# Kernel tuning notes

Hardware: AMD Instinct MI355X
Metric: run time of the kernel (lower is better)

Reference implementation:

```python
import jax, jax.numpy as jnp
import numpy as np

DIM = 2048
NUM_HEADS = 16
HEAD_DIM = 128
SEQ = 4096
HDIM = NUM_HEADS * HEAD_DIM
EPS = 1e-6


def _rope_tables(seq_len, head_dim):
    quarter = head_dim // 4
    ang = (1.0 / 1024.0) ** np.linspace(0.0, 1.0, quarter, dtype=np.float32)
    ang = np.concatenate([ang, np.zeros(quarter, dtype=np.float32)])  # [head_dim//2]
    theta = np.arange(seq_len, dtype=np.float32)[:, None] * ang[None, :]  # [T, D/2]
    return jnp.asarray(np.cos(theta)), jnp.asarray(np.sin(theta))


def _rms_norm(x):
    return x * jax.lax.rsqrt(jnp.mean(x * x, axis=-1, keepdims=True) + EPS)


def _apply_rope(x, cos, sin):
    # x: [B, T, H, D]; cos/sin: [T, D/2]
    c = cos[None, :, None, :]
    s = sin[None, :, None, :]
    x1, x2 = jnp.split(x, 2, axis=-1)
    return jnp.concatenate([x1 * c + x2 * s, -x1 * s + x2 * c], axis=-1)


def setup_inputs() -> dict:
    key = jax.random.key(0)
    k1, k2, k3, k4, k5 = jax.random.split(key, 5)
    x = jax.random.normal(k1, (1, SEQ, DIM), dtype=jnp.float32)
    ve = jax.random.normal(k2, (1, SEQ, HDIM), dtype=jnp.float32)
    lambdas = jax.random.uniform(k3, (2,), dtype=jnp.float32)
    bound = (3.0 ** 0.5) * 0.5 * DIM ** (-0.5)
    qkv_w = jax.random.uniform(k4, (3, HDIM, DIM), dtype=jnp.float32, minval=-bound, maxval=bound)
    proj_w = 0.02 * jax.random.normal(k5, (DIM, HDIM), dtype=jnp.float32)
    return {"x": x, "ve": ve, "lambdas": lambdas, "qkv_w": qkv_w, "proj_w": proj_w}


def reference(x, ve, lambdas, qkv_w, proj_w):
    B, T, _ = x.shape
    cos, sin = _rope_tables(T, HEAD_DIM)
    # fused QKV projection: qkv_w [3, hdim, dim]
    qkv = jnp.einsum('btd,ced->cbte', x, qkv_w)  # [3, B, T, hdim]
    q, k, v = [a.reshape(B, T, NUM_HEADS, HEAD_DIM) for a in qkv]
    q = _apply_rope(_rms_norm(q), cos, sin)
    k = _apply_rope(_rms_norm(k), cos, sin)
    v = lambdas[0] * v + lambdas[1] * ve.reshape(v.shape)
    # causal SDPA, default scale 1/sqrt(head_dim)
    scale = 1.0 / jnp.sqrt(jnp.float32(HEAD_DIM))
    scores = jnp.einsum('bthd,bshd->bhts', q, k) * scale  # [B, H, T, T]
    causal = jnp.tril(jnp.ones((T, T), dtype=bool))
    scores = jnp.where(causal[None, None], scores, jnp.float32(-1e30))
    probs = jax.nn.softmax(scores, axis=-1)
    out = jnp.einsum('bhts,bshd->bthd', probs, v).reshape(B, T, HDIM)
    return out @ proj_w.T
```

## Files before the change

### kernel.cpp

```cpp
#include <hip/hip_runtime.h>
#include <cstdint>
#include <cstddef>

constexpr int T_SEQ = 4096;
constexpr int NH    = 16;
constexpr int HD    = 128;
constexpr int DIM   = 2048;
constexpr int HDIM  = 2048;

typedef __attribute__((ext_vector_type(8)))  short  short8;
typedef __attribute__((ext_vector_type(4)))  float  f32x4;
typedef __attribute__((ext_vector_type(16))) float  f32x16;
typedef __attribute__((ext_vector_type(8)))  unsigned short u16x8;
typedef __attribute__((ext_vector_type(4)))  unsigned short u16x4;
typedef __attribute__((ext_vector_type(4)))  unsigned uint4v;
typedef __attribute__((ext_vector_type(2)))  int int2v;

__device__ __forceinline__ unsigned short f2bf(float f) {
  unsigned u = __float_as_uint(f);
  return (unsigned short)((u + 0x7FFFu + ((u >> 16) & 1u)) >> 16);
}
__device__ __forceinline__ float bf2f(unsigned short h) {
  return __uint_as_float(((unsigned)h) << 16);
}
__device__ __forceinline__ void gload_lds16(const void* g, void* l) {
  __builtin_amdgcn_global_load_lds((const __attribute__((address_space(1))) void*)g,
                                   (__attribute__((address_space(3))) void*)l, 16, 0, 0);
}
__device__ __forceinline__ int2v plswap(int a, int b) {
  return __builtin_amdgcn_permlane32_swap(a, b, false, false);
}
__device__ __forceinline__ void bar() {
  asm volatile("" ::: "memory");
  __builtin_amdgcn_s_barrier();
  asm volatile("" ::: "memory");
}
#define VMCNT(n) asm volatile("s_waitcnt vmcnt(" #n ")" ::: "memory")

__global__ __launch_bounds__(256) void cvt_f32_bf16(const float* __restrict__ in,
                                                    unsigned short* __restrict__ out, int n4) {
  int i = blockIdx.x * 256 + threadIdx.x;
  if (i < n4) {
    float4 v = ((const float4*)in)[i];
    u16x4 o; o.x = f2bf(v.x); o.y = f2bf(v.y); o.z = f2bf(v.z); o.w = f2bf(v.w);
    ((u16x4*)out)[i] = o;
  }
}

__global__ __launch_bounds__(256) void rope_tables(float* __restrict__ cosT, float* __restrict__ sinT) {
  int idx = blockIdx.x * 256 + threadIdx.x;
  if (idx >= T_SEQ * 64) return;
  int t = idx >> 6, i = idx & 63;
  float ang = (i < 32) ? exp2f(-10.0f * (float)i / 31.0f) : 0.0f;
  float th = (float)t * ang;
  cosT[idx] = cosf(th);
  sinT[idx] = sinf(th);
}

template <int MODE>
__global__ __launch_bounds__(512) void gemm256(const unsigned short* __restrict__ A,
                                               const unsigned short* __restrict__ B,
                                               int K, unsigned short* __restrict__ outb,
                                               float* __restrict__ outf, int N) {
  __shared__ __align__(16) char SM[3 * 49152];
  const int tid = threadIdx.x, w = tid >> 6, lane = tid & 63;
  const int wm = w >> 2, wn = w & 3;
  const int lr = lane >> 4, lc = lane & 15, lc7 = lc & 7;
  const int cpx = gridDim.x >> 3;
  const int idx = (blockIdx.x & 7) * cpx + (blockIdx.x >> 3);
  const int m0 = (idx & 31) * 128, n0 = (idx >> 5) * 256;

  const int arow = lane >> 3;
  const int xcol = ((lane & 7) ^ ((lane >> 3) & 7)) * 8;

  auto stageA = [&](int buf, int t) {
    char* base = SM + buf * 49152;
#pragma unroll
    for (int i = 0; i < 2; i++) {
      int c = w + i * 8;
      gload_lds16(A + (size_t)(m0 + c * 8 + arow) * K + t * 64 + xcol, base + c * 1024);
    }
  };
  auto stageB0 = [&](int buf, int t) {
    char* base = SM + buf * 49152 + 16384;
    gload_lds16(B + (size_t)(n0 + w * 8 + arow) * K + t * 64 + xcol, base + w * 1024);
  };
  auto stageB1 = [&](int buf, int t) {
    char* base = SM + buf * 49152 + 16384;
#pragma unroll
    for (int i = 1; i < 4; i++) {
      int c = w + i * 8;
      gload_lds16(B + (size_t)(n0 + c * 8 + arow) * K + t * 64 + xcol, base + c * 1024);
    }
  };

  f32x4 acc[4][4] = {};
  const int NT = K >> 6;

  stageA(0, 0); stageB0(0, 0); stageB1(0, 0);
  stageA(1, 1); stageB0(1, 1); stageB1(1, 1);
  VMCNT(6);
  bar();

#pragma unroll 1
  for (int t = 0; t < NT; t++) {
    const int c = t % 3, s = (t + 2) % 3;
    const bool st = (t + 2) < NT;
    const char* Ab = SM + c * 49152;
    const char* Bb = Ab + 16384;

    short8 a[4], b[4];
#pragma unroll
    for (int mi = 0; mi < 4; mi++)
      a[mi] = *(const short8*)(Ab + (wm * 64 + mi * 16 + lc) * 128 + ((0 + lr) ^ lc7) * 16);
#pragma unroll
    for (int ni = 0; ni < 4; ni++)
      b[ni] = *(const short8*)(Bb + (wn * 64 + ni * 16 + lc) * 128 + ((0 + lr) ^ lc7) * 16);
    if (st) { stageA(s, t + 2); stageB0(s, t + 2); }
    bar();
    __builtin_amdgcn_s_setprio(1);
#pragma unroll
    for (int mi = 0; mi < 4; mi++)
#pragma unroll
      for (int ni = 0; ni < 4; ni++)
        acc[mi][ni] = __builtin_amdgcn_mfma_f32_16x16x32_bf16(a[mi], b[ni], acc[mi][ni], 0, 0, 0);
    __builtin_amdgcn_s_setprio(0);
    bar();

#pragma unroll
    for (int mi = 0; mi < 4; mi++)
      a[mi] = *(const short8*)(Ab + (wm * 64 + mi * 16 + lc) * 128 + ((4 + lr) ^ lc7) * 16);
#pragma unroll
    for (int ni = 0; ni < 4; ni++)
      b[ni] = *(const short8*)(Bb + (wn * 64 + ni * 16 + lc) * 128 + ((4 + lr) ^ lc7) * 16);
    if (st) stageB1(s, t + 2);
    if (st) { VMCNT(6); } else { VMCNT(0); }
    bar();
    __builtin_amdgcn_s_setprio(1);
#pragma unroll
    for (int mi = 0; mi < 4; mi++)
#pragma unroll
      for (int ni = 0; ni < 4; ni++)
        acc[mi][ni] = __builtin_amdgcn_mfma_f32_16x16x32_bf16(a[mi], b[ni], acc[mi][ni], 0, 0, 0);
    __builtin_amdgcn_s_setprio(0);
    bar();
  }

#pragma unroll
  for (int mi = 0; mi < 4; mi++)
#pragma unroll
    for (int ni = 0; ni < 4; ni++)
#pragma unroll
      for (int r = 0; r < 4; r++) {
        int t = m0 + wm * 64 + mi * 16 + lr * 4 + r;
        int n = n0 + wn * 64 + ni * 16 + lc;
        float v = acc[mi][ni][r];
        if (MODE == 0) {
          int cc = n >> 11, e = n & 2047, h = e >> 7, d = e & 127;
          outb[(((size_t)cc * NH + h) * T_SEQ + t) * HD + d] = f2bf(v);
        } else {
          outf[(size_t)t * N + n] = v;
        }
      }
}

__global__ __launch_bounds__(256) void norm_rope(unsigned short* __restrict__ qkvb,
                                                 const float* __restrict__ cosT,
                                                 const float* __restrict__ sinT) {
  const int tid = threadIdx.x;
  const int li = tid & 15;
  const int row = blockIdx.x * 16 + (tid >> 4);
  const int t = row & (T_SEQ - 1);
  unsigned short* rp = qkvb + (size_t)row * HD + li * 8;
  u16x8 raw = *(const u16x8*)rp;

  float v[8]; float ss = 0.0f;
#pragma unroll
  for (int j = 0; j < 8; j++) { v[j] = bf2f(raw[j]); ss += v[j] * v[j]; }
#pragma unroll
  for (int off = 1; off < 16; off <<= 1) ss += __shfl_xor(ss, off, 16);
  float rs = rsqrtf(ss * (1.0f / 128.0f) + 1e-6f);
  if (row < NH * T_SEQ) rs *= 0.088388347648318447f * 1.44269504f;

  uint4v rw = __builtin_bit_cast(uint4v, raw);
  uint4v pwv;
  pwv.x = (unsigned)__shfl_xor((int)rw.x, 8, 16);
  pwv.y = (unsigned)__shfl_xor((int)rw.y, 8, 16);
  pwv.z = (unsigned)__shfl_xor((int)rw.z, 8, 16);
  pwv.w = (unsigned)__shfl_xor((int)rw.w, 8, 16);
  u16x8 praw = __builtin_bit_cast(u16x8, pwv);
  float pv[8];
#pragma unroll
  for (int j = 0; j < 8; j++) pv[j] = bf2f(praw[j]);

  const int e0 = (li & 7) * 8;
  const bool hi8 = li >= 8;
  float4 c0 = *(const float4*)(cosT + t * 64 + e0);
  float4 c1 = *(const float4*)(cosT + t * 64 + e0 + 4);
  float4 s0 = *(const float4*)(sinT + t * 64 + e0);
  float4 s1 = *(const float4*)(sinT + t * 64 + e0 + 4);
  float cc[8] = {c0.x, c0.y, c0.z, c0.w, c1.x, c1.y, c1.z, c1.w};
  float sn[8] = {s0.x, s0.y, s0.z, s0.w, s1.x, s1.y, s1.z, s1.w};

  u16x8 o;
#pragma unroll
  for (int j = 0; j < 8; j++) {
    float x1 = hi8 ? pv[j] : v[j];
    float x2 = hi8 ? v[j] : pv[j];
    float r = hi8 ? (-x1 * sn[j] + x2 * cc[j]) : (x1 * cc[j] + x2 * sn[j]);
    o[j] = f2bf(r * rs);
  }
  *(u16x8*)rp = o;
}

__global__ __launch_bounds__(256) void vmix_transpose(const unsigned short* __restrict__ vb,
                                                      const float* __restrict__ ve,
                                                      const float* __restrict__ lam,
                                                      unsigned short* __restrict__ vt) {
  __shared__ float tile[64][65];
  const int h = blockIdx.z, t0 = blockIdx.x * 64, d0 = blockIdx.y * 64;
  const float l0 = lam[0], l1 = lam[1];
  const int tid = threadIdx.x;
  const int tl = tid >> 4, dl4 = (tid & 15) * 4;
#pragma unroll
  for (int i = 0; i < 4; i++) {
    int t_local = tl + i * 16;
    int t = t0 + t_local;
    const unsigned short* vp = vb + ((size_t)h * T_SEQ + t) * HD + d0 + dl4;
    const float* vep = ve + (size_t)t * HDIM + h * HD + d0 + dl4;
    u16x4 vv = *(const u16x4*)vp;
    float4 vef = *(const float4*)vep;
    tile[t_local][dl4 + 0] = l0 * bf2f(vv.x) + l1 * vef.x;
    tile[t_local][dl4 + 1] = l0 * bf2f(vv.y) + l1 * vef.y;
    tile[t_local][dl4 + 2] = l0 * bf2f(vv.z) + l1 * vef.z;
    tile[t_local][dl4 + 3] = l0 * bf2f(vv.w) + l1 * vef.w;
  }
  __syncthreads();
#pragma unroll
  for (int i = 0; i < 2; i++) {
    int idx = tid + i * 256;
    int d_local = idx >> 3, tloc = (idx & 7) * 8;
    u16x8 o;
#pragma unroll
    for (int j = 0; j < 8; j++) o[j] = f2bf(tile[tloc + j][d_local]);
    *(u16x8*)(vt + ((size_t)h * HD + d0 + d_local) * T_SEQ + t0 + tloc) = o;
  }
}

__global__ __launch_bounds__(512)
__attribute__((amdgpu_waves_per_eu(2, 2)))
void attn_fwd(const unsigned short* __restrict__ qb,
              const unsigned short* __restrict__ kb,
              const unsigned short* __restrict__ vt,
              unsigned short* __restrict__ ao) {
  __shared__ __align__(16) char SMEM[131072];
  __shared__ int gctr[2];
  const int bid = blockIdx.x;
  const int h  = (bid & 7) + ((bid >> 7) << 3);
  const int pr = (bid >> 3) & 15;
  const int tid = threadIdx.x, w = tid >> 6, lane = tid & 63;
  const int g = w >> 2, wq = w & 3;
  const int l31 = lane & 31, hi = lane >> 5, r7 = l31 & 7;
  const unsigned short* qh = qb + (size_t)h * T_SEQ * HD;
  const unsigned short* kh = kb + (size_t)h * T_SEQ * HD;
  const unsigned short* vh = vt + (size_t)h * HD * T_SEQ;

  if (tid < 2) gctr[tid] = 0;
  __syncthreads();
  int bcnt = 0;
  auto GBAR = [&]() {
    asm volatile("s_waitcnt lgkmcnt(0)" ::: "memory");
    ++bcnt;
    if (lane == 0)
      __hip_atomic_fetch_add(&gctr[g], 1, __ATOMIC_RELEASE, __HIP_MEMORY_SCOPE_WORKGROUP);
    while (__hip_atomic_load(&gctr[g], __ATOMIC_ACQUIRE, __HIP_MEMORY_SCOPE_WORKGROUP) < 4 * bcnt)
      __builtin_amdgcn_s_sleep(1);
  };

  char* Kbase = SMEM + g * 65536;
  char* Vbase = SMEM + g * 65536 + 32768;

  const int kcrow = lane >> 4, kcol16 = lane & 15;
  const int vcrow = lane >> 3, vslot0 = lane & 7;

  auto STAGE = [&](int buf, int t) {
#pragma unroll
    for (int i = 0; i < 4; i++) {
      int krow = (wq * 4 + i) * 4 + kcrow;
      int kcol = (kcol16 ^ (krow & 7)) * 8;
      gload_lds16(kh + (size_t)(t * 64 + krow) * HD + kcol,
                  Kbase + buf * 16384 + (wq * 4 + i) * 1024);
      int vrow = (wq * 4 + i) * 8 + vcrow;
      int vcol = (vslot0 ^ (vrow & 7)) * 8;
      gload_lds16(vh + (size_t)vrow * T_SEQ + t * 64 + vcol,
                  Vbase + buf * 16384 + (wq * 4 + i) * 1024);
    }
  };

  const float FM = 16.5f;

#pragma unroll 1
  for (int which = 0; which < 2; ++which) {
    const int qt = which ? pr : (31 - pr);
    const int ng = qt + 1;
    const int q_row = qt * 128 + wq * 32 + l31;

    short8 qf[8];
#pragma unroll
    for (int dk = 0; dk < 8; dk++)
      qf[dk] = *(const short8*)(qh + (size_t)q_row * HD + dk * 16 + hi * 8);

    f32x16 accO[4] = {};
    float l_r = 0.0f;

    __syncthreads();
    STAGE(0, g);

#pragma unroll 1
    for (int it = 0; it < ng; it++) {
      const int t = 2 * it + g;
      const int cur = it & 1;
      asm volatile("s_waitcnt vmcnt(0)" ::: "memory");
      GBAR();
      if (it + 1 < ng) STAGE(cur ^ 1, t + 2);

      f32x16 accS0 = {}, accS1 = {};
      const char* Kb = Kbase + cur * 16384 + l31 * 256;
      __builtin_amdgcn_s_setprio(1);
#pragma unroll
      for (int dk = 0; dk < 8; dk++) {
        int sl = ((2 * dk + hi) ^ r7) * 16;
        short8 k0 = *(const short8*)(Kb + sl);
        short8 k1 = *(const short8*)(Kb + 32 * 256 + sl);
        accS0 = __builtin_amdgcn_mfma_f32_32x32x16_bf16(k0, qf[dk], accS0, 0, 0, 0);
        accS1 = __builtin_amdgcn_mfma_f32_32x32x16_bf16(k1, qf[dk], accS1, 0, 0, 0);
      }
      __builtin_amdgcn_s_setprio(0);

      float p[32];
      const bool need_mask = (t * 64 + 63) > (qt * 128 + wq * 32);
      if (need_mask) {
#pragma unroll
        for (int r = 0; r < 16; r++) {
          int kv0 = t * 64 + (r & 3) + 8 * (r >> 2) + 4 * hi;
          p[r]      = (kv0      > q_row) ? 0.0f : exp2f(accS0[r] - FM);
          p[16 + r] = (kv0 + 32 > q_row) ? 0.0f : exp2f(accS1[r] - FM);
        }
      } else {
#pragma unroll
        for (int r = 0; r < 16; r++) {
          p[r]      = exp2f(accS0[r] - FM);
          p[16 + r] = exp2f(accS1[r] - FM);
        }
      }

      float s16[16];
#pragma unroll
      for (int i = 0; i < 16; i++) s16[i] = p[i] + p[i + 16];
#pragma unroll
      for (int st = 8; st >= 1; st >>= 1)
#pragma unroll
        for (int i = 0; i < st; i++) s16[i] += s16[i + st];
      int2v sr_ = plswap(__float_as_int(s16[0]), __float_as_int(s16[0]));
      l_r += s16[0] + __int_as_float(hi ? sr_.x : sr_.y);

      unsigned pk[8][2];
#pragma unroll
      for (int o = 0; o < 8; o++)
#pragma unroll
        for (int c = 0; c < 2; c++) {
          float lo = p[(o >> 2) * 16 + (o & 3) * 4 + 2 * c];
          float hi_ = p[(o >> 2) * 16 + (o & 3) * 4 + 2 * c + 1];
          asm("v_cvt_pk_bf16_f32 %0, %1, %2" : "=v"(pk[o][c]) : "v"(lo), "v"(hi_));
        }

      const char* Vb = Vbase + cur * 16384 + l31 * 128;
#pragma unroll
      for (int ks = 0; ks < 4; ks++) {
        int2v s0 = plswap((int)pk[2 * ks][0], (int)pk[2 * ks + 1][0]);
        int2v s1 = plswap((int)pk[2 * ks][1], (int)pk[2 * ks + 1][1]);
        uint4v pw;
        pw.x = (unsigned)s0.x;
        pw.y = (unsigned)s1.x;
        pw.z = (unsigned)s0.y;
        pw.w = (unsigned)s1.y;
        short8 pb = __builtin_bit_cast(short8, pw);
        int sl = ((2 * ks + hi) ^ r7) * 16;
        __builtin_amdgcn_s_setprio(1);
#pragma unroll
        for (int dt = 0; dt < 4; dt++) {
          short8 vf = *(const short8*)(Vb + dt * 32 * 128 + sl);
          accO[dt] = __builtin_amdgcn_mfma_f32_32x32x16_bf16(vf, pb, accO[dt], 0, 0, 0);
        }
        __builtin_amdgcn_s_setprio(0);
      }
    }

    __syncthreads();
    float* SM_acc = (float*)(SMEM + 65536);
    float* SM_l   = (float*)SMEM;
    const int q_local = wq * 32 + l31;
    if (g == 1) {
#pragma unroll
      for (int dt = 0; dt < 4; dt++)
#pragma unroll
        for (int r = 0; r < 16; r++) {
          int d = 32 * dt + (r & 3) + 8 * (r >> 2) + 4 * hi;
          SM_acc[q_local * 128 + (d ^ l31)] = accO[dt][r];
        }
      if (hi == 0) SM_l[q_local] = l_r;
    }
    __syncthreads();
    if (g == 0) {
      float lo = SM_l[q_local];
      float inv = 1.0f / (l_r + lo);
#pragma unroll
      for (int dt = 0; dt < 4; dt++)
#pragma unroll
        for (int q4 = 0; q4 < 4; q4++) {
          int dbase = 32 * dt + 8 * q4 + 4 * hi;
          u16x4 o;
#pragma unroll
          for (int j = 0; j < 4; j++) {
            int r = q4 * 4 + j, d = dbase + j;
            float vo = SM_acc[q_local * 128 + (d ^ l31)];
            o[j] = f2bf((accO[dt][r] + vo) * inv);
          }
          *(u16x4*)(ao + (size_t)q_row * HDIM + h * HD + dbase) = o;
        }
    }
  }
}

extern "C" void kernel_launch(void* const* d_in, const int* in_sizes, int n_in,
                              void* d_out, int out_size, void* d_ws, size_t ws_size,
                              hipStream_t stream) {
  const float* x      = (const float*)d_in[0];
  const float* ve     = (const float*)d_in[1];
  const float* lam    = (const float*)d_in[2];
  const float* qkv_w  = (const float*)d_in[3];
  const float* proj_w = (const float*)d_in[4];
  float* out = (float*)d_out;

  char* p = (char*)d_ws;
  float* cosT = (float*)p;            p += (size_t)T_SEQ * 64 * 4;
  float* sinT = (float*)p;            p += (size_t)T_SEQ * 64 * 4;
  unsigned short* xb   = (unsigned short*)p; p += (size_t)T_SEQ * DIM * 2;
  unsigned short* wqb  = (unsigned short*)p; p += (size_t)3 * HDIM * DIM * 2;
  unsigned short* pwb  = (unsigned short*)p; p += (size_t)DIM * HDIM * 2;
  unsigned short* qkvb = (unsigned short*)p; p += (size_t)3 * NH * T_SEQ * HD * 2;
  unsigned short* vtb  = (unsigned short*)p; p += (size_t)NH * HD * T_SEQ * 2;
  unsigned short* aob  = (unsigned short*)p; p += (size_t)T_SEQ * HDIM * 2;

  cvt_f32_bf16<<<(T_SEQ * DIM / 4 + 255) / 256, 256, 0, stream>>>(x, xb, T_SEQ * DIM / 4);
  cvt_f32_bf16<<<(3 * HDIM * DIM / 4 + 255) / 256, 256, 0, stream>>>(qkv_w, wqb, 3 * HDIM * DIM / 4);
  cvt_f32_bf16<<<(DIM * HDIM / 4 + 255) / 256, 256, 0, stream>>>(proj_w, pwb, DIM * HDIM / 4);
  rope_tables<<<(T_SEQ * 64 + 255) / 256, 256, 0, stream>>>(cosT, sinT);

  gemm256<0><<<768, 512, 0, stream>>>(xb, wqb, DIM, qkvb, nullptr, 3 * HDIM);
  norm_rope<<<2 * NH * T_SEQ / 16, 256, 0, stream>>>(qkvb, cosT, sinT);
  vmix_transpose<<<dim3(T_SEQ / 64, HD / 64, NH), 256, 0, stream>>>(
      qkvb + (size_t)2 * NH * T_SEQ * HD, ve, lam, vtb);
  attn_fwd<<<256, 512, 0, stream>>>(qkvb, qkvb + (size_t)NH * T_SEQ * HD, vtb, aob);
  gemm256<1><<<256, 512, 0, stream>>>(aob, pwb, HDIM, nullptr, out, HDIM);
}
```

Measured before the change: 327.9 us.

## Fuse prep kernels and permute K rows to drop permlane swaps in attention

Merges the three fp32-to-bf16 conversion launches and the RoPE table launch into one prep kernel, removing three kernel launches. In attention, K rows are loaded into LDS in a permuted order, so the score accumulator layout already matches the B-operand layout needed for the P·V MFMA. This removes the permlane32 swaps and the separate pack step, and the causal mask index is updated to match the new row order. The risk is a mismatch between the mask index formula and the new K row permutation.

```diff
diff --git a/kernel.cpp b/kernel.cpp
--- a/kernel.cpp
+++ b/kernel.cpp
@@ -37,24 +37,34 @@
 }
 #define VMCNT(n) asm volatile("s_waitcnt vmcnt(" #n ")" ::: "memory")
 
-__global__ __launch_bounds__(256) void cvt_f32_bf16(const float* __restrict__ in,
-                                                    unsigned short* __restrict__ out, int n4) {
-  int i = blockIdx.x * 256 + threadIdx.x;
-  if (i < n4) {
-    float4 v = ((const float4*)in)[i];
-    u16x4 o; o.x = f2bf(v.x); o.y = f2bf(v.y); o.z = f2bf(v.z); o.w = f2bf(v.w);
-    ((u16x4*)out)[i] = o;
-  }
-}
-
-__global__ __launch_bounds__(256) void rope_tables(float* __restrict__ cosT, float* __restrict__ sinT) {
-  int idx = blockIdx.x * 256 + threadIdx.x;
-  if (idx >= T_SEQ * 64) return;
-  int t = idx >> 6, i = idx & 63;
-  float ang = (i < 32) ? exp2f(-10.0f * (float)i / 31.0f) : 0.0f;
-  float th = (float)t * ang;
-  cosT[idx] = cosf(th);
-  sinT[idx] = sinf(th);
+__global__ __launch_bounds__(256) void prep_all(const float* __restrict__ x,
+                                                const float* __restrict__ qkv_w,
+                                                const float* __restrict__ proj_w,
+                                                unsigned short* __restrict__ xb,
+                                                unsigned short* __restrict__ wqb,
+                                                unsigned short* __restrict__ pwb,
+                                                float* __restrict__ cosT,
+                                                float* __restrict__ sinT) {
+  constexpr int N1 = T_SEQ * DIM / 4;
+  constexpr int N2 = N1 + 3 * HDIM * DIM / 4;
+  constexpr int N3 = N2 + DIM * HDIM / 4;
+  int gid = blockIdx.x * 256 + threadIdx.x;
+  const float* src; unsigned short* dst; int i4;
+  if (gid < N1)      { src = x;      dst = xb;  i4 = gid; }
+  else if (gid < N2) { src = qkv_w;  dst = wqb; i4 = gid - N1; }
+  else if (gid < N3) { src = proj_w; dst = pwb; i4 = gid - N2; }
+  else {
+    int idx = gid - N3;
+    int t = idx >> 6, i = idx & 63;
+    float ang = (i < 32) ? exp2f(-10.0f * (float)i / 31.0f) : 0.0f;
+    float th = (float)t * ang;
+    cosT[idx] = cosf(th);
+    sinT[idx] = sinf(th);
+    return;
+  }
+  float4 v = ((const float4*)src)[i4];
+  u16x4 o; o.x = f2bf(v.x); o.y = f2bf(v.y); o.z = f2bf(v.z); o.w = f2bf(v.w);
+  ((u16x4*)dst)[i4] = o;
 }
 
 template <int MODE>
@@ -287,8 +297,9 @@
 #pragma unroll
     for (int i = 0; i < 4; i++) {
       int krow = (wq * 4 + i) * 4 + kcrow;
+      int ksrc = (krow & ~12) | ((krow & 4) << 1) | ((krow & 8) >> 1);
       int kcol = (kcol16 ^ (krow & 7)) * 8;
-      gload_lds16(kh + (size_t)(t * 64 + krow) * HD + kcol,
+      gload_lds16(kh + (size_t)(t * 64 + ksrc) * HD + kcol,
                   Kbase + buf * 16384 + (wq * 4 + i) * 1024);
       int vrow = (wq * 4 + i) * 8 + vcrow;
       int vcol = (vslot0 ^ (vrow & 7)) * 8;
@@ -342,7 +353,7 @@
       if (need_mask) {
 #pragma unroll
         for (int r = 0; r < 16; r++) {
-          int kv0 = t * 64 + (r & 3) + 8 * (r >> 2) + 4 * hi;
+          int kv0 = t * 64 + (r & 7) + 8 * hi + 16 * (r >> 3);
           p[r]      = (kv0      > q_row) ? 0.0f : exp2f(accS0[r] - FM);
           p[16 + r] = (kv0 + 32 > q_row) ? 0.0f : exp2f(accS1[r] - FM);
         }
@@ -364,26 +375,17 @@
       int2v sr_ = plswap(__float_as_int(s16[0]), __float_as_int(s16[0]));
       l_r += s16[0] + __int_as_float(hi ? sr_.x : sr_.y);
 
-      unsigned pk[8][2];
-#pragma unroll
-      for (int o = 0; o < 8; o++)
-#pragma unroll
-        for (int c = 0; c < 2; c++) {
-          float lo = p[(o >> 2) * 16 + (o & 3) * 4 + 2 * c];
-          float hi_ = p[(o >> 2) * 16 + (o & 3) * 4 + 2 * c + 1];
-          asm("v_cvt_pk_bf16_f32 %0, %1, %2" : "=v"(pk[o][c]) : "v"(lo), "v"(hi_));
-        }
-
       const char* Vb = Vbase + cur * 16384 + l31 * 128;
 #pragma unroll
       for (int ks = 0; ks < 4; ks++) {
-        int2v s0 = plswap((int)pk[2 * ks][0], (int)pk[2 * ks + 1][0]);
-        int2v s1 = plswap((int)pk[2 * ks][1], (int)pk[2 * ks + 1][1]);
         uint4v pw;
-        pw.x = (unsigned)s0.x;
-        pw.y = (unsigned)s1.x;
-        pw.z = (unsigned)s0.y;
-        pw.w = (unsigned)s1.y;
+#pragma unroll
+        for (int w2 = 0; w2 < 4; w2++) {
+          unsigned pk_;
+          asm("v_cvt_pk_bf16_f32 %0, %1, %2"
+              : "=v"(pk_) : "v"(p[8 * ks + 2 * w2]), "v"(p[8 * ks + 2 * w2 + 1]));
+          pw[w2] = pk_;
+        }
         short8 pb = __builtin_bit_cast(short8, pw);
         int sl = ((2 * ks + hi) ^ r7) * 16;
         __builtin_amdgcn_s_setprio(1);
@@ -452,10 +454,8 @@
   unsigned short* vtb  = (unsigned short*)p; p += (size_t)NH * HD * T_SEQ * 2;
   unsigned short* aob  = (unsigned short*)p; p += (size_t)T_SEQ * HDIM * 2;
 
-  cvt_f32_bf16<<<(T_SEQ * DIM / 4 + 255) / 256, 256, 0, stream>>>(x, xb, T_SEQ * DIM / 4);
-  cvt_f32_bf16<<<(3 * HDIM * DIM / 4 + 255) / 256, 256, 0, stream>>>(qkv_w, wqb, 3 * HDIM * DIM / 4);
-  cvt_f32_bf16<<<(DIM * HDIM / 4 + 255) / 256, 256, 0, stream>>>(proj_w, pwb, DIM * HDIM / 4);
-  rope_tables<<<(T_SEQ * 64 + 255) / 256, 256, 0, stream>>>(cosT, sinT);
+  constexpr int PREP_N = T_SEQ * DIM / 4 + 3 * HDIM * DIM / 4 + DIM * HDIM / 4 + T_SEQ * 64;
+  prep_all<<<PREP_N / 256, 256, 0, stream>>>(x, qkv_w, proj_w, xb, wqb, pwb, cosT, sinT);
 
   gemm256<0><<<768, 512, 0, stream>>>(xb, wqb, DIM, qkvb, nullptr, 3 * HDIM);
   norm_rope<<<2 * NH * T_SEQ / 16, 256, 0, stream>>>(qkvb, cosT, sinT);
```

Measured after the change: 319.9 us. -2.4%, faster.
